# Kernel optimization log

Measured on AMD Instinct MI355X. Metric: run time of the kernel, lower is better.

## Reference

```python
import jax, jax.numpy as jnp
from jax import lax
import numpy as np

# Model dims (from MambaVisionEncoder defaults + HF MambaConfig defaults)
HIDDEN = 128      # hidden_dim
DEPTH = 4         # num_hidden_layers
INTER = 4 * HIDDEN  # intermediate_size = 512
STATE = 16        # state_size
DT_RANK = 8       # ceil(hidden/16)
KCONV = 4         # conv_kernel
EPS = 1e-5        # layer_norm_epsilon
B_, T_ = 2, 256
C_, H_, W_ = 3, 224, 224
INPUT_DIM = C_ * H_ * W_


def setup_inputs() -> dict:
    key = jax.random.key(0)
    ks = jax.random.split(key, 8)
    s = 0.02
    return {
        "x": jax.random.normal(ks[0], (B_, T_, C_, H_, W_), jnp.float32),
        # torch Linear weights are [out, in]
        "project_w": jax.random.normal(ks[1], (HIDDEN, INPUT_DIM), jnp.float32) * s,
        "project_b": jnp.zeros((HIDDEN,), jnp.float32),
        "in_proj_w": jax.random.normal(ks[2], (DEPTH, 2 * INTER, HIDDEN), jnp.float32) * s,
        "conv_w": jax.random.normal(ks[3], (DEPTH, INTER, KCONV), jnp.float32) * s,
        "conv_b": jnp.zeros((DEPTH, INTER), jnp.float32),
        "x_proj_w": jax.random.normal(ks[4], (DEPTH, DT_RANK + 2 * STATE, INTER), jnp.float32) * s,
        "dt_proj_w": jax.random.normal(ks[5], (DEPTH, INTER, DT_RANK), jnp.float32) * s,
        "dt_proj_b": jnp.zeros((DEPTH, INTER), jnp.float32),
        # S4D-style init: A_log = log(1..N), broadcast over channels
        "A_log": jnp.log(jnp.broadcast_to(jnp.arange(1, STATE + 1, dtype=jnp.float32), (DEPTH, INTER, STATE))),
        "D_ssm": jnp.ones((DEPTH, INTER), jnp.float32),
        "out_proj_w": jax.random.normal(ks[6], (DEPTH, HIDDEN, INTER), jnp.float32) * s,
        "norm_w": jnp.ones((DEPTH, HIDDEN), jnp.float32),
        "norm_f_w": jnp.ones((HIDDEN,), jnp.float32),
    }


def rmsnorm(x, w):
    var = jnp.mean(jnp.square(x), axis=-1, keepdims=True)
    return x * lax.rsqrt(var + EPS) * w


def mamba_mixer(h, ipw, cw, cb, xpw, dtw, dtb, A_log, Dp, opw):
    # h: [B, T, D]
    Bsz, T, _ = h.shape
    proj = jnp.einsum('btd,ed->bte', h, ipw)          # [B, T, 2I]
    hs, gate = jnp.split(proj, 2, axis=-1)
    hs = hs.transpose(0, 2, 1)                         # [B, I, T]
    # causal depthwise conv1d, kernel KCONV
    conv = lax.conv_general_dilated(
        hs, cw[:, None, :], (1,), [(KCONV - 1, 0)],
        dimension_numbers=('NCH', 'OIH', 'NCH'), feature_group_count=INTER)
    hs = jax.nn.silu(conv + cb[None, :, None])         # [B, I, T]
    ssm_in = jnp.einsum('bit,ei->bte', hs, xpw)        # [B, T, dt_rank+2N]
    dt, Bm, Cm = jnp.split(ssm_in, [DT_RANK, DT_RANK + STATE], axis=-1)
    dt = jax.nn.softplus(jnp.einsum('btr,ir->bti', dt, dtw) + dtb)  # [B, T, I]
    A = -jnp.exp(A_log)                                # [I, N]
    u = hs.transpose(0, 2, 1)                          # [B, T, I]
    dA = jnp.exp(dt[..., None] * A[None, None])        # [B, T, I, N]
    dBu = dt[..., None] * Bm[:, :, None, :] * u[..., None]  # [B, T, I, N]

    def step(state, inp):                              # state: [B, I, N]
        dA_t, dBu_t, C_t = inp
        state = dA_t * state + dBu_t
        y_t = jnp.einsum('bin,bn->bi', state, C_t)
        return state, y_t

    init = jnp.zeros((Bsz, INTER, STATE), hs.dtype)
    _, ys = lax.scan(step, init, (dA.transpose(1, 0, 2, 3), dBu.transpose(1, 0, 2, 3), Cm.transpose(1, 0, 2)))
    y = ys.transpose(1, 0, 2)                          # [B, T, I]
    y = (y + u * Dp[None, None, :]) * jax.nn.silu(gate)
    return jnp.einsum('bti,di->btd', y, opw)           # [B, T, D]


def reference(x, project_w, project_b, in_proj_w, conv_w, conv_b, x_proj_w,
              dt_proj_w, dt_proj_b, A_log, D_ssm, out_proj_w, norm_w, norm_f_w):
    B, T = x.shape[0], x.shape[1]
    flat = x.reshape(B, T, -1)                         # [B, T, input_dim]
    h = jnp.einsum('bti,di->btd', flat, project_w) + project_b  # [B, T, HIDDEN]
    for l in range(DEPTH):
        h = h + mamba_mixer(rmsnorm(h, norm_w[l]), in_proj_w[l], conv_w[l], conv_b[l],
                            x_proj_w[l], dt_proj_w[l], dt_proj_b[l], A_log[l],
                            D_ssm[l], out_proj_w[l])
    return rmsnorm(h, norm_f_w)
```

## Files before the change

kernel.cpp:

```cpp
#include <hip/hip_runtime.h>
#include <hip/hip_bf16.h>

#define HIDDEN 128
#define DEPTH 4
#define INTER 512
#define NSTATE 16
#define DT_RANK 8
#define EPS_RMS 1e-5f
#define MTOK 512
#define KIN 150528

typedef __attribute__((ext_vector_type(8))) short bf16x8;
typedef __attribute__((ext_vector_type(4))) float f32x4;

__device__ __forceinline__ unsigned short f2bf(float f) {
  unsigned int u = __builtin_bit_cast(unsigned int, f);
  u += 0x7fffu + ((u >> 16) & 1u);
  return (unsigned short)(u >> 16);
}
__device__ __forceinline__ float silu_f(float x) {
  return x / (1.0f + __expf(-x));
}

__global__ __launch_bounds__(256) void zero_part(float* __restrict__ p)
{
  const size_t i = (size_t)blockIdx.x * 256 + threadIdx.x;
  ((float4*)p)[i] = (float4){0.f, 0.f, 0.f, 0.f};
}

__global__ __launch_bounds__(512) void proj_gemm(
    const float* __restrict__ x, const float* __restrict__ w,
    float* __restrict__ partial)
{
  const int bid = blockIdx.x;
  const int nslab = 18 + (bid < 96 ? 1 : 0);
  const int s0 = bid * 18 + (bid < 96 ? bid : 96);
  __shared__ unsigned short xs[512 * 32];
  __shared__ unsigned short wsm[128 * 32];
  const int tid = threadIdx.x;
  const int lane = tid & 63;
  const int wv = tid >> 6;
  const int fr = lane & 15;
  const int kg = (lane >> 4) * 8;
  const int r8 = tid >> 3;
  const int c4 = (tid & 7) * 4;

  f32x4 acc[4][8];
  #pragma unroll
  for (int mi = 0; mi < 4; ++mi)
    #pragma unroll
    for (int ni = 0; ni < 8; ++ni)
      acc[mi][ni] = (f32x4){0.f, 0.f, 0.f, 0.f};

  float4 rx[8], rw[2];
  {
    const float* xk = x + (size_t)s0 * 32 + c4;
    const float* wk = w + (size_t)s0 * 32 + c4;
    #pragma unroll
    for (int p = 0; p < 8; ++p) rx[p] = *(const float4*)(xk + (size_t)(r8 + p * 64) * KIN);
    #pragma unroll
    for (int p = 0; p < 2; ++p) rw[p] = *(const float4*)(wk + (size_t)(r8 + p * 64) * KIN);
  }

  for (int ks = 0; ks < nslab; ++ks) {
    #pragma unroll
    for (int p = 0; p < 8; ++p) {
      ushort4 bx = {f2bf(rx[p].x), f2bf(rx[p].y), f2bf(rx[p].z), f2bf(rx[p].w)};
      *(ushort4*)&xs[(r8 + p * 64) * 32 + c4] = bx;
    }
    #pragma unroll
    for (int p = 0; p < 2; ++p) {
      ushort4 bw = {f2bf(rw[p].x), f2bf(rw[p].y), f2bf(rw[p].z), f2bf(rw[p].w)};
      *(ushort4*)&wsm[(r8 + p * 64) * 32 + c4] = bw;
    }
    __syncthreads();
    if (ks < nslab - 1) {
      const float* xk = x + (size_t)(s0 + ks + 1) * 32 + c4;
      const float* wk = w + (size_t)(s0 + ks + 1) * 32 + c4;
      #pragma unroll
      for (int p = 0; p < 8; ++p) rx[p] = *(const float4*)(xk + (size_t)(r8 + p * 64) * KIN);
      #pragma unroll
      for (int p = 0; p < 2; ++p) rw[p] = *(const float4*)(wk + (size_t)(r8 + p * 64) * KIN);
    }
    bf16x8 a[4];
    #pragma unroll
    for (int mi = 0; mi < 4; ++mi)
      a[mi] = *(const bf16x8*)&xs[(wv * 64 + mi * 16 + fr) * 32 + kg];
    #pragma unroll
    for (int ni = 0; ni < 8; ++ni) {
      const bf16x8 bfr = *(const bf16x8*)&wsm[(ni * 16 + fr) * 32 + kg];
      #pragma unroll
      for (int mi = 0; mi < 4; ++mi)
        acc[mi][ni] = __builtin_amdgcn_mfma_f32_16x16x32_bf16(a[mi], bfr, acc[mi][ni], 0, 0, 0);
    }
    __syncthreads();
  }
  float* hp = partial + (size_t)(bid & 7) * (MTOK * HIDDEN);
  #pragma unroll
  for (int mi = 0; mi < 4; ++mi)
    #pragma unroll
    for (int ni = 0; ni < 8; ++ni)
      #pragma unroll
      for (int r = 0; r < 4; ++r) {
        const int grow = wv * 64 + mi * 16 + (lane >> 4) * 4 + r;
        const int gcol = ni * 16 + fr;
        atomicAdd(hp + (size_t)grow * HIDDEN + gcol, acc[mi][ni][r]);
      }
}

__global__ __launch_bounds__(512) void fusedA(
    int mode,
    const float* __restrict__ part, const float* __restrict__ pb,
    const float* __restrict__ y_g, const float* __restrict__ gate_g,
    float* __restrict__ h_g,
    const float* __restrict__ opw,
    const float* __restrict__ nw,
    const float* __restrict__ ipw,
    float* __restrict__ hs_g, float* __restrict__ gate_out,
    float* __restrict__ dout)
{
  const int m0 = blockIdx.x * 2;
  const int tid = threadIdx.x;
  const int o2 = tid >> 1;
  const int half = tid & 1;
  const int t = o2 >> 7, d = o2 & 127;
  __shared__ float y2[2][512];
  __shared__ float hrow[2][128];
  __shared__ float hn[2][128];

  float hv;
  if (mode == 0) {
    hv = pb[d];
    #pragma unroll
    for (int s = 0; s < 8; ++s)
      hv += part[(size_t)s * (MTOK * HIDDEN) + (size_t)(m0 + t) * 128 + d];
  } else {
    #pragma unroll
    for (int j = 0; j < 2; ++j) {
      const int o = tid + j * 512;
      const int tt = o >> 9, i = o & 511;
      const float yv = y_g[(size_t)(m0 + tt) * 512 + i];
      const float g  = gate_g[(size_t)(m0 + tt) * 512 + i];
      y2[tt][i] = yv * silu_f(g);
    }
    __syncthreads();
    const float4* yp = (const float4*)(&y2[t][0] + half * 256);
    const float4* wp = (const float4*)(opw + (size_t)d * 512 + half * 256);
    float a0 = 0.f, a1 = 0.f, a2 = 0.f, a3 = 0.f;
    #pragma unroll 8
    for (int kk = 0; kk < 64; ++kk) {
      const float4 yv = yp[kk], wv4 = wp[kk];
      a0 += yv.x * wv4.x; a1 += yv.y * wv4.y;
      a2 += yv.z * wv4.z; a3 += yv.w * wv4.w;
    }
    float a = (a0 + a1) + (a2 + a3);
    a += __shfl_xor(a, 1);
    hv = h_g[(size_t)(m0 + t) * 128 + d] + a;
  }
  if (mode != 2 && half == 0) h_g[(size_t)(m0 + t) * 128 + d] = hv;
  if (half == 0) hrow[t][d] = hv;
  __syncthreads();
  {
    const int wvi = tid >> 6, ln = tid & 63;
    const int tt = wvi & 1;
    const float v0 = hrow[tt][ln], v1 = hrow[tt][ln + 64];
    float ss = v0 * v0 + v1 * v1;
    #pragma unroll
    for (int off = 1; off < 64; off <<= 1) ss += __shfl_xor(ss, off);
    const float rr = rsqrtf(ss * (1.0f / 128.0f) + EPS_RMS);
    if (mode == 2) {
      if (wvi < 2) {
        dout[(size_t)(m0 + tt) * 128 + ln]      = v0 * rr * nw[ln];
        dout[(size_t)(m0 + tt) * 128 + ln + 64] = v1 * rr * nw[ln + 64];
      }
      return;
    }
    if (wvi < 2) {
      hn[tt][ln]      = v0 * rr * nw[ln];
      hn[tt][ln + 64] = v1 * rr * nw[ln + 64];
    }
  }
  __syncthreads();
  #pragma unroll
  for (int j = 0; j < 4; ++j) {
    const int o = tid + j * 512;
    const int tt = o >> 10, e = o & 1023;
    const float4* hp4 = (const float4*)&hn[tt][0];
    const float4* wp4 = (const float4*)(ipw + (size_t)e * 128);
    float a0 = 0.f, a1 = 0.f, a2 = 0.f, a3 = 0.f;
    #pragma unroll
    for (int kk = 0; kk < 32; ++kk) {
      const float4 hvv = hp4[kk], wv4 = wp4[kk];
      a0 += hvv.x * wv4.x; a1 += hvv.y * wv4.y;
      a2 += hvv.z * wv4.z; a3 += hvv.w * wv4.w;
    }
    const float a = (a0 + a1) + (a2 + a3);
    if (e < 512) hs_g[(size_t)(m0 + tt) * 512 + e] = a;
    else         gate_out[(size_t)(m0 + tt) * 512 + (e - 512)] = a;
  }
}

__global__ __launch_bounds__(512) void convxp(
    const float* __restrict__ hs_g, const float* __restrict__ cw,
    const float* __restrict__ cb, const float* __restrict__ xpw,
    const float* __restrict__ dtw, const float* __restrict__ dtb,
    float* __restrict__ uT, float* __restrict__ dtT,
    float* __restrict__ Bm, float* __restrict__ Cm)
{
  const int m0 = blockIdx.x * 2;
  const int b = m0 >> 8, tb0 = m0 & 255;
  const int tid = threadIdx.x;
  __shared__ float hs5[5][512];
  __shared__ float u4[2][512];
  __shared__ float si[2][40];
  for (int o = tid; o < 2560; o += 512) {
    const int j = o >> 9, i = o & 511;
    const int ct = tb0 - 3 + j;
    hs5[j][i] = (ct >= 0) ? hs_g[((size_t)b * 256 + ct) * 512 + i] : 0.f;
  }
  __syncthreads();
  #pragma unroll
  for (int j = 0; j < 2; ++j) {
    const int o = tid + j * 512;
    const int t = o >> 9, i = o & 511;
    const float4 c4v = *(const float4*)(cw + (size_t)i * 4);
    const float s = cb[i] + c4v.x * hs5[t][i] + c4v.y * hs5[t + 1][i]
                          + c4v.z * hs5[t + 2][i] + c4v.w * hs5[t + 3][i];
    const float uu = silu_f(s);
    u4[t][i] = uu;
    uT[((size_t)b * 512 + i) * 256 + tb0 + t] = uu;
  }
  __syncthreads();
  if (tid < 160) {
    const int pid = tid >> 1, half = tid & 1;
    const int t = pid / 40, e = pid % 40;
    const float4* up = (const float4*)(&u4[t][0] + half * 256);
    const float4* wp = (const float4*)(xpw + (size_t)e * 512 + half * 256);
    float a0 = 0.f, a1 = 0.f, a2 = 0.f, a3 = 0.f;
    #pragma unroll 8
    for (int kk = 0; kk < 64; ++kk) {
      const float4 uv = up[kk], wv4 = wp[kk];
      a0 += uv.x * wv4.x; a1 += uv.y * wv4.y;
      a2 += uv.z * wv4.z; a3 += uv.w * wv4.w;
    }
    float a = (a0 + a1) + (a2 + a3);
    a += __shfl_xor(a, 1);
    if (half == 0) si[t][e] = a;
  }
  __syncthreads();
  if (tid < 64) {
    const int t = tid >> 5, q = tid & 31;
    if (q < 16) Bm[(size_t)(m0 + t) * 16 + q] = si[t][8 + q];
    else        Cm[(size_t)(m0 + t) * 16 + (q - 16)] = si[t][24 + (q - 16)];
  }
  #pragma unroll
  for (int j = 0; j < 2; ++j) {
    const int o = tid + j * 512;
    const int i = o >> 1, t = o & 1;
    float a0 = dtb[i];
    const float* dr = dtw + (size_t)i * 8;
    #pragma unroll
    for (int r = 0; r < 8; ++r) a0 += si[t][r] * dr[r];
    const float sp = (a0 > 20.f) ? a0 : log1pf(__expf(a0));
    dtT[((size_t)b * 512 + i) * 256 + tb0 + t] = sp;
  }
}

__global__ __launch_bounds__(256) void scan_k(
    const float* __restrict__ uT, const float* __restrict__ dtT,
    const float* __restrict__ Bm, const float* __restrict__ Cm,
    const float* __restrict__ Alog, const float* __restrict__ Dssm,
    float* __restrict__ y_g)
{
  const int blk = blockIdx.x;
  const int b = blk >> 9, i = blk & 511;
  const int tid = threadIdx.x;
  __shared__ float dt_r[256], u_r[256];
  __shared__ float B_l[256][17], C_l[256][17];
  __shared__ float e_l[16][17], P_l[16][17];
  dt_r[tid] = dtT[((size_t)b * 512 + i) * 256 + tid];
  u_r[tid]  = uT[((size_t)b * 512 + i) * 256 + tid];
  #pragma unroll
  for (int j = 0; j < 16; ++j) {
    const int o = tid + j * 256;
    B_l[o >> 4][o & 15] = Bm[(size_t)b * 4096 + o];
    C_l[o >> 4][o & 15] = Cm[(size_t)b * 4096 + o];
  }
  __syncthreads();
  const int c = tid >> 4, n = tid & 15;
  const float Av = -__expf(Alog[(size_t)i * 16 + n]);
  const float Dv = Dssm[i];
  float aj[16], xj[16];
  float s = 0.f, P = 1.f;
  #pragma unroll
  for (int j = 0; j < 16; ++j) {
    const int t = c * 16 + j;
    const float dtv = dt_r[t];
    const float a = __expf(Av * dtv);
    const float xx = dtv * B_l[t][n] * u_r[t];
    aj[j] = a; xj[j] = xx;
    s = a * s + xx; P *= a;
  }
  e_l[c][n] = s; P_l[c][n] = P;
  __syncthreads();
  float s0 = 0.f;
  for (int cc = 0; cc < c; ++cc)
    s0 = P_l[cc][n] * s0 + e_l[cc][n];
  s = s0;
  #pragma unroll
  for (int j = 0; j < 16; ++j) {
    const int t = c * 16 + j;
    s = aj[j] * s + xj[j];
    float p = s * C_l[t][n];
    p += __shfl_xor(p, 1); p += __shfl_xor(p, 2);
    p += __shfl_xor(p, 4); p += __shfl_xor(p, 8);
    if (n == 0)
      y_g[((size_t)b * 256 + t) * 512 + i] = p + u_r[t] * Dv;
  }
}

extern "C" void kernel_launch(void* const* d_in, const int* in_sizes, int n_in,
                              void* d_out, int out_size, void* d_ws, size_t ws_size,
                              hipStream_t stream)
{
  (void)in_sizes; (void)n_in; (void)out_size; (void)ws_size;
  const float* x    = (const float*)d_in[0];
  const float* pw   = (const float*)d_in[1];
  const float* pb   = (const float*)d_in[2];
  const float* ipw  = (const float*)d_in[3];
  const float* cw   = (const float*)d_in[4];
  const float* cb   = (const float*)d_in[5];
  const float* xpw  = (const float*)d_in[6];
  const float* dtw  = (const float*)d_in[7];
  const float* dtb  = (const float*)d_in[8];
  const float* Alog = (const float*)d_in[9];
  const float* Dssm = (const float*)d_in[10];
  const float* opw  = (const float*)d_in[11];
  const float* nw   = (const float*)d_in[12];
  const float* nwf  = (const float*)d_in[13];
  float* out = (float*)d_out;

  float* ws   = (float*)d_ws;
  float* part = ws;
  float* h    = part + 8 * 65536;
  float* hs   = h + 65536;
  float* gate = hs + 262144;
  float* uT   = gate + 262144;
  float* dtT  = uT + 262144;
  float* Bm   = dtT + 262144;
  float* Cm   = Bm + 8192;
  float* y    = Cm + 8192;

  zero_part<<<dim3(512), 256, 0, stream>>>(part);
  proj_gemm<<<dim3(256), 512, 0, stream>>>(x, pw, part);

  fusedA<<<dim3(256), 512, 0, stream>>>(0, part, pb, nullptr, nullptr, h,
                                        nullptr, nw, ipw, hs, gate, nullptr);
  for (int l = 0; l < DEPTH; ++l) {
    convxp<<<dim3(256), 512, 0, stream>>>(
        hs, cw + (size_t)l * 2048, cb + (size_t)l * 512,
        xpw + (size_t)l * 40 * 512, dtw + (size_t)l * 512 * 8,
        dtb + (size_t)l * 512, uT, dtT, Bm, Cm);
    scan_k<<<dim3(1024), 256, 0, stream>>>(
        uT, dtT, Bm, Cm, Alog + (size_t)l * 512 * 16, Dssm + (size_t)l * 512, y);
    if (l < DEPTH - 1)
      fusedA<<<dim3(256), 512, 0, stream>>>(1, nullptr, nullptr, y, gate, h,
          opw + (size_t)l * 128 * 512, nw + (size_t)(l + 1) * 128,
          ipw + (size_t)(l + 1) * 1024 * 128, hs, gate, nullptr);
    else
      fusedA<<<dim3(256), 512, 0, stream>>>(2, nullptr, nullptr, y, gate, h,
          opw + (size_t)l * 128 * 512, nwf, nullptr, nullptr, nullptr, out);
  }
}
```

Baseline: 448.9 us.

## Retile projection GEMM into M×K blocks with wider K chunks and swizzled LDS

The large input projection GEMM is repartitioned so each block handles a 128-row M tile over a K range, instead of all 512 rows over a K slab. Each K chunk is widened to 128 elements with an XOR-swizzled LDS layout to avoid bank conflicts. Waves are arranged 2×4 over the M/N tile, and the partial-sum buffer grows from 8 to 16 slices to spread atomics. This is meant to improve global load coalescing (512B contiguous per row) and LDS efficiency. In exchange the weight matrix is re-read once per M tile, and the reduction in the following kernel sums more partials.

```diff
diff --git a/kernel.cpp b/kernel.cpp
--- a/kernel.cpp
+++ b/kernel.cpp
@@ -33,78 +33,87 @@
     float* __restrict__ partial)
 {
   const int bid = blockIdx.x;
-  const int nslab = 18 + (bid < 96 ? 1 : 0);
-  const int s0 = bid * 18 + (bid < 96 ? bid : 96);
-  __shared__ unsigned short xs[512 * 32];
-  __shared__ unsigned short wsm[128 * 32];
+  const int mb = (bid >> 3) & 3;
+  const int kb = (bid & 7) + (bid >> 5) * 8;
+  const int nchunk = 18 + (kb < 24 ? 1 : 0);
+  const int c0 = kb * 18 + (kb < 24 ? kb : 24);
+
+  __shared__ char sm[256 * 256];
+
   const int tid = threadIdx.x;
   const int lane = tid & 63;
   const int wv = tid >> 6;
+  const int wm2 = wv >> 2;
+  const int wn4 = wv & 3;
   const int fr = lane & 15;
-  const int kg = (lane >> 4) * 8;
-  const int r8 = tid >> 3;
-  const int c4 = (tid & 7) * 4;
-
-  f32x4 acc[4][8];
+  const int kq = lane >> 4;
+  const int l31 = lane & 31;
+  const int rpar = lane >> 5;
+
+  const float* gptr = (wv < 4)
+      ? (x + (size_t)(mb * 128 + wv * 32 + rpar) * KIN + l31 * 4)
+      : (w + (size_t)((wv - 4) * 32 + rpar) * KIN + l31 * 4);
+
+  f32x4 acc[4][2];
+  #pragma unroll
+  for (int mi = 0; mi < 4; ++mi) {
+    acc[mi][0] = (f32x4){0.f, 0.f, 0.f, 0.f};
+    acc[mi][1] = (f32x4){0.f, 0.f, 0.f, 0.f};
+  }
+
+  float4 rv[16];
+  {
+    const float* base = gptr + (size_t)c0 * 128;
+    #pragma unroll
+    for (int j = 0; j < 16; ++j)
+      rv[j] = *(const float4*)(base + (size_t)(j * 2) * KIN);
+  }
+
+  for (int cc = 0; cc < nchunk; ++cc) {
+    #pragma unroll
+    for (int j = 0; j < 16; ++j) {
+      const int r = wv * 32 + j * 2 + rpar;
+      const int phys = (l31 * 8) ^ ((r & 7) << 4);
+      ushort4 bq = {f2bf(rv[j].x), f2bf(rv[j].y), f2bf(rv[j].z), f2bf(rv[j].w)};
+      *(ushort4*)(sm + r * 256 + phys) = bq;
+    }
+    __syncthreads();
+    if (cc + 1 < nchunk) {
+      const float* base = gptr + (size_t)(c0 + cc + 1) * 128;
+      #pragma unroll
+      for (int j = 0; j < 16; ++j)
+        rv[j] = *(const float4*)(base + (size_t)(j * 2) * KIN);
+    }
+    #pragma unroll
+    for (int ks = 0; ks < 4; ++ks) {
+      const int log = ks * 64 + kq * 16;
+      bf16x8 a[4];
+      #pragma unroll
+      for (int mi = 0; mi < 4; ++mi) {
+        const int row = wm2 * 64 + mi * 16 + fr;
+        a[mi] = *(const bf16x8*)(sm + row * 256 + (log ^ ((row & 7) << 4)));
+      }
+      #pragma unroll
+      for (int ni = 0; ni < 2; ++ni) {
+        const int row = 128 + wn4 * 32 + ni * 16 + fr;
+        const bf16x8 b = *(const bf16x8*)(sm + row * 256 + (log ^ ((row & 7) << 4)));
+        #pragma unroll
+        for (int mi = 0; mi < 4; ++mi)
+          acc[mi][ni] = __builtin_amdgcn_mfma_f32_16x16x32_bf16(a[mi], b, acc[mi][ni], 0, 0, 0);
+      }
+    }
+    __syncthreads();
+  }
+  float* hp = partial + (size_t)(kb & 15) * (MTOK * HIDDEN);
   #pragma unroll
   for (int mi = 0; mi < 4; ++mi)
     #pragma unroll
-    for (int ni = 0; ni < 8; ++ni)
-      acc[mi][ni] = (f32x4){0.f, 0.f, 0.f, 0.f};
-
-  float4 rx[8], rw[2];
-  {
-    const float* xk = x + (size_t)s0 * 32 + c4;
-    const float* wk = w + (size_t)s0 * 32 + c4;
-    #pragma unroll
-    for (int p = 0; p < 8; ++p) rx[p] = *(const float4*)(xk + (size_t)(r8 + p * 64) * KIN);
-    #pragma unroll
-    for (int p = 0; p < 2; ++p) rw[p] = *(const float4*)(wk + (size_t)(r8 + p * 64) * KIN);
-  }
-
-  for (int ks = 0; ks < nslab; ++ks) {
-    #pragma unroll
-    for (int p = 0; p < 8; ++p) {
-      ushort4 bx = {f2bf(rx[p].x), f2bf(rx[p].y), f2bf(rx[p].z), f2bf(rx[p].w)};
-      *(ushort4*)&xs[(r8 + p * 64) * 32 + c4] = bx;
-    }
-    #pragma unroll
-    for (int p = 0; p < 2; ++p) {
-      ushort4 bw = {f2bf(rw[p].x), f2bf(rw[p].y), f2bf(rw[p].z), f2bf(rw[p].w)};
-      *(ushort4*)&wsm[(r8 + p * 64) * 32 + c4] = bw;
-    }
-    __syncthreads();
-    if (ks < nslab - 1) {
-      const float* xk = x + (size_t)(s0 + ks + 1) * 32 + c4;
-      const float* wk = w + (size_t)(s0 + ks + 1) * 32 + c4;
-      #pragma unroll
-      for (int p = 0; p < 8; ++p) rx[p] = *(const float4*)(xk + (size_t)(r8 + p * 64) * KIN);
-      #pragma unroll
-      for (int p = 0; p < 2; ++p) rw[p] = *(const float4*)(wk + (size_t)(r8 + p * 64) * KIN);
-    }
-    bf16x8 a[4];
-    #pragma unroll
-    for (int mi = 0; mi < 4; ++mi)
-      a[mi] = *(const bf16x8*)&xs[(wv * 64 + mi * 16 + fr) * 32 + kg];
-    #pragma unroll
-    for (int ni = 0; ni < 8; ++ni) {
-      const bf16x8 bfr = *(const bf16x8*)&wsm[(ni * 16 + fr) * 32 + kg];
-      #pragma unroll
-      for (int mi = 0; mi < 4; ++mi)
-        acc[mi][ni] = __builtin_amdgcn_mfma_f32_16x16x32_bf16(a[mi], bfr, acc[mi][ni], 0, 0, 0);
-    }
-    __syncthreads();
-  }
-  float* hp = partial + (size_t)(bid & 7) * (MTOK * HIDDEN);
-  #pragma unroll
-  for (int mi = 0; mi < 4; ++mi)
-    #pragma unroll
-    for (int ni = 0; ni < 8; ++ni)
+    for (int ni = 0; ni < 2; ++ni)
       #pragma unroll
       for (int r = 0; r < 4; ++r) {
-        const int grow = wv * 64 + mi * 16 + (lane >> 4) * 4 + r;
-        const int gcol = ni * 16 + fr;
-        atomicAdd(hp + (size_t)grow * HIDDEN + gcol, acc[mi][ni][r]);
+        const int row = mb * 128 + wm2 * 64 + mi * 16 + kq * 4 + r;
+        const int col = wn4 * 32 + ni * 16 + fr;
+        atomicAdd(hp + (size_t)row * HIDDEN + col, acc[mi][ni][r]);
       }
 }
 
@@ -132,7 +141,7 @@
   if (mode == 0) {
     hv = pb[d];
     #pragma unroll
-    for (int s = 0; s < 8; ++s)
+    for (int s = 0; s < 16; ++s)
       hv += part[(size_t)s * (MTOK * HIDDEN) + (size_t)(m0 + t) * 128 + d];
   } else {
     #pragma unroll
@@ -342,7 +351,7 @@
 
   float* ws   = (float*)d_ws;
   float* part = ws;
-  float* h    = part + 8 * 65536;
+  float* h    = part + 16 * 65536;
   float* hs   = h + 65536;
   float* gate = hs + 262144;
   float* uT   = gate + 262144;
@@ -351,7 +360,7 @@
   float* Cm   = Bm + 8192;
   float* y    = Cm + 8192;
 
-  zero_part<<<dim3(512), 256, 0, stream>>>(part);
+  zero_part<<<dim3(1024), 256, 0, stream>>>(part);
   proj_gemm<<<dim3(256), 512, 0, stream>>>(x, pw, part);
 
   fusedA<<<dim3(256), 512, 0, stream>>>(0, part, pb, nullptr, nullptr, h,
```

Result: faster. 415.5 us (-7.4%).
